# Optimization experiments

Hardware: AMD Instinct MI355X
Metric: run time of the kernel (lower is better)

Reference implementation:

```python
import jax, jax.numpy as jnp
import numpy as np

SEQ_LEN = 20   # fixed by the 18/19/20-position loop in get_each_word_feature
EMB = 768
FEAT = 512
EPS = 1e-12    # F.normalize eps


def _conv_relu(x, W, b):
    # x: [bs, L, 768]; W: [K, 768, C]; b: [C]
    # Equivalent to Conv2d(1, C, (K, 768)) on x.unsqueeze(1), then ReLU+squeeze.
    K = W.shape[0]
    L = x.shape[1]
    out = b
    for j in range(K):  # K in {1,2,3}: tiny static loop
        out = out + jnp.einsum('bld,dc->blc', x[:, j:L - K + 1 + j], W[j])
    return jax.nn.relu(out)  # [bs, L-K+1, C]


def _l2norm(x, axis):
    n = jnp.sqrt(jnp.sum(x * x, axis=axis, keepdims=True))
    return x / jnp.maximum(n, EPS)


def setup_inputs() -> dict:
    key = jax.random.key(0)
    ks = jax.random.split(key, 10)
    bs = 4096
    s = 0.02
    return {
        'words_emb': jax.random.normal(ks[0], (bs, SEQ_LEN, EMB), jnp.float32),
        'sent_emb': jax.random.normal(ks[1], (bs, EMB), jnp.float32),
        'W1': jax.random.normal(ks[2], (1, EMB, FEAT), jnp.float32) * s,
        'b1': jnp.zeros((FEAT,), jnp.float32),
        'W2': jax.random.normal(ks[3], (2, EMB, FEAT), jnp.float32) * s,
        'b2': jnp.zeros((FEAT,), jnp.float32),
        'W3': jax.random.normal(ks[4], (3, EMB, FEAT), jnp.float32) * s,
        'b3': jnp.zeros((FEAT,), jnp.float32),
        'Wp': jax.random.normal(ks[5], (EMB, FEAT), jnp.float32) * s,
        'bp': jnp.zeros((FEAT,), jnp.float32),
    }


def reference(words_emb, sent_emb, W1, b1, W2, b2, W3, b3, Wp, bp):
    # sentence projection (ProjectionHead.forward applies only the Linear)
    sent = sent_emb @ Wp + bp                       # [bs, C]

    # Bert_Word_Mapping: three 1D convs over tokens, kernel widths 1/2/3
    a = _conv_relu(words_emb, W1, b1)               # [bs, 20, C]
    b_ = _conv_relu(words_emb, W2, b2)              # [bs, 19, C]
    c = _conv_relu(words_emb, W3, b3)               # [bs, 18, C]

    # get_each_word_feature, vectorized: positional max over available convs.
    # ReLU outputs are >= 0, so zero-padding short sequences makes the
    # elementwise max reproduce the original per-position stack+amax exactly.
    b_pad = jnp.pad(b_, ((0, 0), (0, 1), (0, 0)))   # [bs, 20, C]
    c_pad = jnp.pad(c, ((0, 0), (0, 2), (0, 0)))    # [bs, 20, C]
    code = jnp.maximum(jnp.maximum(a, b_pad), c_pad)
    code = _l2norm(code, axis=2)                    # normalize over feature dim
    words_out = jnp.transpose(code, (0, 2, 1))      # [bs, C, 20]

    # get_word_feature: global max-pool over token dim, mean of 3, L2 norm
    pooled = (a.max(axis=1) + b_.max(axis=1) + c.max(axis=1)) / 3.0  # [bs, C]
    word_vector = _l2norm(pooled, axis=1)

    return (words_out, word_vector, sent)
```

## Files before the change

kernel.cpp:

```cpp
#include <hip/hip_runtime.h>
#include <hip/hip_bf16.h>
#include <stdint.h>

typedef __bf16 bf16_t;
typedef __bf16 bf16x8 __attribute__((ext_vector_type(8)));
typedef float f32x4 __attribute__((ext_vector_type(4)));

#define BS       4096
#define SEQ      20
#define SEQP     22
#define EMB      768
#define FEAT     512
#define KA       2304
#define WV_BASE   (41943040L)
#define SENT_BASE (44040192L)

#define BT_OFF    0L
#define WPT_OFF   7077888L
#define SENTX_OFF 7864320L
#define XPAD_OFF  14155776L
#define WS_MIN    111673344L
#define WS_FULL   404226048L

__device__ __forceinline__ void async_copy16(void* lds, const void* g) {
  __builtin_amdgcn_global_load_lds(
      (__attribute__((address_space(1))) void*)(void*)g,
      (__attribute__((address_space(3))) void*)lds,
      16, 0, 0);
}

__global__ void pack_xpad(const float* __restrict__ words, bf16_t* __restrict__ Xpad) {
  long idx4 = ((long)blockIdx.x * blockDim.x + threadIdx.x) * 4;
  long row = idx4 / EMB;
  int  d   = (int)(idx4 % EMB);
  long b   = row / SEQP;
  int  r   = (int)(row % SEQP);
  ushort4 o;
  if (r < SEQ) {
    float4 v = *(const float4*)(words + ((b * SEQ + r) * EMB + d));
    o.x = __builtin_bit_cast(unsigned short, (bf16_t)v.x);
    o.y = __builtin_bit_cast(unsigned short, (bf16_t)v.y);
    o.z = __builtin_bit_cast(unsigned short, (bf16_t)v.z);
    o.w = __builtin_bit_cast(unsigned short, (bf16_t)v.w);
  } else {
    o.x = 0; o.y = 0; o.z = 0; o.w = 0;
  }
  *(ushort4*)(&Xpad[idx4]) = o;
}

__global__ void pack_sent(const float* __restrict__ sent, bf16_t* __restrict__ Xs) {
  long idx4 = ((long)blockIdx.x * blockDim.x + threadIdx.x) * 4;
  float4 v = *(const float4*)(sent + idx4);
  ushort4 o;
  o.x = __builtin_bit_cast(unsigned short, (bf16_t)v.x);
  o.y = __builtin_bit_cast(unsigned short, (bf16_t)v.y);
  o.z = __builtin_bit_cast(unsigned short, (bf16_t)v.z);
  o.w = __builtin_bit_cast(unsigned short, (bf16_t)v.w);
  *(ushort4*)(&Xs[idx4]) = o;
}

__global__ void pack_bt(const float* __restrict__ W1, const float* __restrict__ W2,
                        const float* __restrict__ W3, bf16_t* __restrict__ Bt) {
  long idx = (long)blockIdx.x * blockDim.x + threadIdx.x;
  int n = (int)(idx / KA), k = (int)(idx % KA);
  int g = n >> 9, c = n & 511;
  int j = k / EMB, d = k % EMB;
  float v = 0.f;
  if (j <= g) {
    const float* W = (g == 0) ? W1 : ((g == 1) ? W2 : W3);
    v = W[((long)j * EMB + d) * FEAT + c];
  }
  Bt[idx] = (bf16_t)v;
}

__global__ void pack_wpt(const float* __restrict__ Wp, bf16_t* __restrict__ Wpt) {
  long idx = (long)blockIdx.x * blockDim.x + threadIdx.x;
  int n = (int)(idx / EMB), k = (int)(idx % EMB);
  Wpt[idx] = (bf16_t)Wp[(long)k * FEAT + n];
}

__global__ __launch_bounds__(256, 2)
void gemm_sent(const bf16_t* __restrict__ A, const bf16_t* __restrict__ Bt,
               const float* __restrict__ bias, float* __restrict__ S) {
  __shared__ bf16_t As[128 * 64];
  __shared__ bf16_t Bs[128 * 64];

  const int tid  = threadIdx.x;
  const int lane = tid & 63;
  const int w    = tid >> 6;
  const int m0   = blockIdx.x * 128;
  const int n0t  = blockIdx.y * 128;

  long agbase[4], bgbase[4];
  int  ldsoff[4];
  #pragma unroll
  for (int i = 0; i < 4; i++) {
    int r = w * 32 + i * 8 + (lane >> 3);
    int cg = (lane & 7) ^ (r & 7);
    agbase[i] = (long)(m0 + r) * EMB + cg * 8;
    bgbase[i] = (long)(n0t + r) * EMB + cg * 8;
    ldsoff[i] = (w * 32 + i * 8) * 64;
  }

  const int wm = w >> 1, wn = w & 1;
  const int q = lane >> 4, ln = lane & 15;
  int aoff[4][2], boff[4][2];
  #pragma unroll
  for (int t = 0; t < 4; t++) {
    int ra = wm * 64 + t * 16 + ln;
    int rb = wn * 64 + t * 16 + ln;
    #pragma unroll
    for (int ks = 0; ks < 2; ks++) {
      int c = ks * 4 + q;
      aoff[t][ks] = ra * 64 + ((c ^ (ra & 7)) * 8);
      boff[t][ks] = rb * 64 + ((c ^ (rb & 7)) * 8);
    }
  }

  f32x4 acc[4][4];
  #pragma unroll
  for (int i = 0; i < 4; i++)
    #pragma unroll
    for (int j = 0; j < 4; j++) acc[i][j] = (f32x4)0.f;

  for (int kb = 0; kb < EMB; kb += 64) {
    #pragma unroll
    for (int i = 0; i < 4; i++) {
      async_copy16(&As[ldsoff[i]], A  + agbase[i] + kb);
      async_copy16(&Bs[ldsoff[i]], Bt + bgbase[i] + kb);
    }
    __syncthreads();
    #pragma unroll
    for (int ks = 0; ks < 2; ks++) {
      bf16x8 af[4], bfr[4];
      #pragma unroll
      for (int t = 0; t < 4; t++) af[t]  = *(const bf16x8*)&As[aoff[t][ks]];
      #pragma unroll
      for (int t = 0; t < 4; t++) bfr[t] = *(const bf16x8*)&Bs[boff[t][ks]];
      #pragma unroll
      for (int mt = 0; mt < 4; mt++)
        #pragma unroll
        for (int nt = 0; nt < 4; nt++)
          acc[mt][nt] = __builtin_amdgcn_mfma_f32_16x16x32_bf16(af[mt], bfr[nt], acc[mt][nt], 0, 0, 0);
    }
    __syncthreads();
  }

  #pragma unroll
  for (int nt = 0; nt < 4; nt++) {
    int c = n0t + wn * 64 + nt * 16 + ln;
    float bv = bias[c];
    #pragma unroll
    for (int mt = 0; mt < 4; mt++) {
      int mrow = m0 + wm * 64 + mt * 16 + q * 4;
      #pragma unroll
      for (int v = 0; v < 4; v++)
        S[(long)(mrow + v) * FEAT + c] = acc[mt][nt][v] + bv;
    }
  }
}


#define MM4(MH, I, AV)                                                                               \
  acc[(MH)*4+(I)][0] = __builtin_amdgcn_mfma_f32_16x16x32_bf16(AV, b0_, acc[(MH)*4+(I)][0], 0, 0, 0); \
  acc[(MH)*4+(I)][1] = __builtin_amdgcn_mfma_f32_16x16x32_bf16(AV, b1_, acc[(MH)*4+(I)][1], 0, 0, 0); \
  acc[(MH)*4+(I)][2] = __builtin_amdgcn_mfma_f32_16x16x32_bf16(AV, b2_, acc[(MH)*4+(I)][2], 0, 0, 0); \
  acc[(MH)*4+(I)][3] = __builtin_amdgcn_mfma_f32_16x16x32_bf16(AV, b3_, acc[(MH)*4+(I)][3], 0, 0, 0);

#define ARD(MH, AB)                                                  \
    bf16x8 a0_ = *(const bf16x8*)&smem[(AB) + aoff[MH][0]];          \
    bf16x8 a1_ = *(const bf16x8*)&smem[(AB) + aoff[MH][1]];          \
    bf16x8 a2_ = *(const bf16x8*)&smem[(AB) + aoff[MH][2]];          \
    bf16x8 a3_ = *(const bf16x8*)&smem[(AB) + aoff[MH][3]];

#define BRD(BB)                                                      \
    b0_ = *(const bf16x8*)&smem[(BB) + boff[0]];                     \
    b1_ = *(const bf16x8*)&smem[(BB) + boff[1]];                     \
    b2_ = *(const bf16x8*)&smem[(BB) + boff[2]];                     \
    b3_ = *(const bf16x8*)&smem[(BB) + boff[3]];

#define PH_SYNC()                                                    \
    __builtin_amdgcn_s_barrier();                                    \
    asm volatile("s_waitcnt lgkmcnt(0)" ::: "memory");               \
    __builtin_amdgcn_sched_barrier(0);                               \
    __builtin_amdgcn_s_setprio(1)

#define PH_END()                                                     \
    __builtin_amdgcn_s_setprio(0);                                   \
    __builtin_amdgcn_s_barrier()

__global__ __launch_bounds__(512, 2)
void gemm8(const bf16_t* __restrict__ Axp, const bf16_t* __restrict__ Bt,
           const float* __restrict__ bias1, const float* __restrict__ bias2,
           const float* __restrict__ bias3, bf16_t* __restrict__ P, int Mtot) {
  __shared__ bf16_t smem[65536];

  const int tid  = threadIdx.x;
  const int lane = tid & 63, w = tid >> 6;
  const int wm = w >> 2, wn = w & 3;
  const int ln = lane & 15, q = lane >> 4;
  const int wbase = w * 512;

  const int nx   = gridDim.x;
  const int nwg  = nx * 6;
  const int orig = blockIdx.y * nx + blockIdx.x;
  const int wgid = (orig & 7) * (nwg >> 3) + (orig >> 3);
  const int bx = wgid / 6, by = wgid % 6;
  const int m0  = bx * 256;
  const int n0t = by * 256;
  const int g   = by >> 1;
  const int NT  = 12 * (g + 1);

  long aSrc0, aSrc1, bSrc0, bSrc1;
  {
    int pair = (tid >> 3);
    int u    = (tid & 7) ^ (pair & 7);
    int row  = pair * 2 + (u >> 2);
    int c    = u & 3;
    int m    = m0 + row;
    aSrc0 = ((long)(m / SEQ) * SEQP + (m % SEQ)) * EMB + c * 8;
    bSrc0 = (long)(n0t + row) * KA + c * 8;
    pair += 64;
    u   = (tid & 7) ^ (pair & 7);
    row = pair * 2 + (u >> 2);
    c   = u & 3;
    m   = m0 + row;
    aSrc1 = ((long)(m / SEQ) * SEQP + (m % SEQ)) * EMB + c * 8;
    bSrc1 = (long)(n0t + row) * KA + c * 8;
  }

  auto stA = [&](int buf, int ks, int kb) {
    const int rb = buf * 32768 + ks * 8192;
    async_copy16(&smem[rb + wbase],        Axp + aSrc0 + kb + ks * 32);
    async_copy16(&smem[rb + 4096 + wbase], Axp + aSrc1 + kb + ks * 32);
  };
  auto stB = [&](int buf, int ks, int kb) {
    const int rb = buf * 32768 + 16384 + ks * 8192;
    async_copy16(&smem[rb + wbase],        Bt + bSrc0 + kb + ks * 32);
    async_copy16(&smem[rb + 4096 + wbase], Bt + bSrc1 + kb + ks * 32);
  };

  int aoff[2][4], boff[4];
  #pragma unroll
  for (int mh = 0; mh < 2; mh++)
    #pragma unroll
    for (int t4 = 0; t4 < 4; t4++) {
      int r = wm * 128 + mh * 64 + t4 * 16 + ln;
      int slot = (q | ((r & 1) << 2)) ^ ((r >> 1) & 7);
      aoff[mh][t4] = (r >> 1) * 64 + slot * 8;
    }
  #pragma unroll
  for (int nf = 0; nf < 4; nf++) {
    int r = wn * 64 + nf * 16 + ln;
    int slot = (q | ((r & 1) << 2)) ^ ((r >> 1) & 7);
    boff[nf] = (r >> 1) * 64 + slot * 8;
  }

  f32x4 acc[8][4];
  #pragma unroll
  for (int i = 0; i < 8; i++)
    #pragma unroll
    for (int j = 0; j < 4; j++) acc[i][j] = (f32x4)0.f;

  stA(0, 0, 0);
  stA(0, 1, 0);
  stB(0, 0, 0);
  stB(0, 1, 0);
  stB(1, 0, 64);
  stA(1, 0, 64);
  stB(1, 1, 64);
  asm volatile("s_waitcnt vmcnt(6)" ::: "memory");
  __builtin_amdgcn_s_barrier();

  for (int t = 0; t < NT; ++t) {
    const int cb  = (t & 1) << 15;
    const int ab0 = cb, ab1 = cb + 8192;
    const int bb0 = cb + 16384, bb1 = cb + 24576;
    const int nb  = (t & 1) ^ 1;
    bf16x8 b0_, b1_, b2_, b3_;

    {
      ARD(0, ab0)
      BRD(bb0)
      if (t + 1 < NT) stA(nb, 1, (t + 1) * 64);
      PH_SYNC();
      MM4(0, 0, a0_) MM4(0, 1, a1_) MM4(0, 2, a2_) MM4(0, 3, a3_)
      PH_END();
    }
    {
      ARD(1, ab0)
      if (t + 2 < NT) stB(t & 1, 0, (t + 2) * 64);
      PH_SYNC();
      MM4(1, 0, a0_) MM4(1, 1, a1_) MM4(1, 2, a2_) MM4(1, 3, a3_)
      PH_END();
    }
    {
      ARD(0, ab1)
      BRD(bb1)
      if (t + 2 < NT) stA(t & 1, 0, (t + 2) * 64);
      PH_SYNC();
      MM4(0, 0, a0_) MM4(0, 1, a1_) MM4(0, 2, a2_) MM4(0, 3, a3_)
      PH_END();
    }
    {
      ARD(1, ab1)
      if (t + 2 < NT) stB(t & 1, 1, (t + 2) * 64);
      PH_SYNC();
      MM4(1, 0, a0_) MM4(1, 1, a1_) MM4(1, 2, a2_) MM4(1, 3, a3_)
      __builtin_amdgcn_s_setprio(0);
      if (t + 2 < NT)      { asm volatile("s_waitcnt vmcnt(6)" ::: "memory"); }
      else if (t + 1 < NT) { asm volatile("s_waitcnt vmcnt(0)" ::: "memory"); }
      __builtin_amdgcn_s_barrier();
    }
  }

  const float* bias = (g == 0) ? bias1 : ((g == 1) ? bias2 : bias3);
  const int gc0 = (by & 1) * 256;
  #pragma unroll
  for (int nf = 0; nf < 4; nf++) {
    int c = gc0 + wn * 64 + nf * 16 + ln;
    float bv = bias[c];
    #pragma unroll
    for (int mf = 0; mf < 8; mf++) {
      int mrow = m0 + wm * 128 + mf * 16 + q * 4;
      #pragma unroll
      for (int v = 0; v < 4; v++) {
        int m = mrow + v;
        int l = m % SEQ;
        float val = acc[mf][nf][v] + bv;
        val = val > 0.f ? val : 0.f;
        if (l >= SEQ - g) val = 0.f;
        P[((long)g * Mtot + m) * FEAT + c] = (bf16_t)val;
      }
    }
  }
}

__global__ __launch_bounds__(256)
void epilogue_k(const bf16_t* __restrict__ P, float* __restrict__ out, int b0, int Mtot) {
  const int bl = blockIdx.x;
  const long b = b0 + bl;
  const int t = threadIdx.x;
  const int lane = t & 63, w = t >> 6;
  const int c0 = t * 2;

  float code[SEQ][2];
  #pragma unroll
  for (int l = 0; l < SEQ; l++) { code[l][0] = 0.f; code[l][1] = 0.f; }
  float mg[3][2];

  #pragma unroll
  for (int gg = 0; gg < 3; gg++) {
    float mx0 = 0.f, mx1 = 0.f;
    #pragma unroll
    for (int l = 0; l < SEQ; l++) {
      uint32_t u = *(const uint32_t*)&P[((long)gg * Mtot + (long)bl * SEQ + l) * FEAT + c0];
      float v0 = __builtin_bit_cast(float, u << 16);
      float v1 = __builtin_bit_cast(float, u & 0xffff0000u);
      code[l][0] = fmaxf(code[l][0], v0);
      code[l][1] = fmaxf(code[l][1], v1);
      mx0 = fmaxf(mx0, v0); mx1 = fmaxf(mx1, v1);
    }
    mg[gg][0] = mx0; mg[gg][1] = mx1;
  }

  __shared__ float red[SEQ][4];
  __shared__ float redp[4];

  #pragma unroll
  for (int l = 0; l < SEQ; l++) {
    float s = code[l][0] * code[l][0] + code[l][1] * code[l][1];
    #pragma unroll
    for (int off = 32; off; off >>= 1) s += __shfl_xor(s, off, 64);
    if (lane == 0) red[l][w] = s;
  }
  float p0 = (mg[0][0] + mg[1][0] + mg[2][0]) * (1.f / 3.f);
  float p1 = (mg[0][1] + mg[1][1] + mg[2][1]) * (1.f / 3.f);
  float sp = p0 * p0 + p1 * p1;
  #pragma unroll
  for (int off = 32; off; off >>= 1) sp += __shfl_xor(sp, off, 64);
  if (lane == 0) redp[w] = sp;
  __syncthreads();

  float rnorm[SEQ];
  #pragma unroll
  for (int l = 0; l < SEQ; l++) {
    float s = red[l][0] + red[l][1] + red[l][2] + red[l][3];
    rnorm[l] = 1.f / fmaxf(sqrtf(s), 1e-12f);
  }
  float sP = redp[0] + redp[1] + redp[2] + redp[3];
  float rnp = 1.f / fmaxf(sqrtf(sP), 1e-12f);

  #pragma unroll
  for (int cc = 0; cc < 2; cc++) {
    long base = b * (FEAT * SEQ) + (long)(c0 + cc) * SEQ;
    #pragma unroll
    for (int l0 = 0; l0 < SEQ; l0 += 4) {
      float4 v;
      v.x = code[l0 + 0][cc] * rnorm[l0 + 0];
      v.y = code[l0 + 1][cc] * rnorm[l0 + 1];
      v.z = code[l0 + 2][cc] * rnorm[l0 + 2];
      v.w = code[l0 + 3][cc] * rnorm[l0 + 3];
      *(float4*)&out[base + l0] = v;
    }
  }
  out[WV_BASE + b * FEAT + c0]     = p0 * rnp;
  out[WV_BASE + b * FEAT + c0 + 1] = p1 * rnp;
}

extern "C" void kernel_launch(void* const* d_in, const int* in_sizes, int n_in,
                              void* d_out, int out_size, void* d_ws, size_t ws_size,
                              hipStream_t stream) {
  const float* words = (const float*)d_in[0];
  const float* sent  = (const float*)d_in[1];
  const float* W1 = (const float*)d_in[2];
  const float* b1 = (const float*)d_in[3];
  const float* W2 = (const float*)d_in[4];
  const float* b2 = (const float*)d_in[5];
  const float* W3 = (const float*)d_in[6];
  const float* b3 = (const float*)d_in[7];
  const float* Wp = (const float*)d_in[8];
  const float* bp = (const float*)d_in[9];
  float* out = (float*)d_out;
  char* ws = (char*)d_ws;

  int CBr, NCH;
  if (ws_size >= (size_t)WS_FULL)     { CBr = 4096; NCH = 1; }
  else if (ws_size >= (size_t)WS_MIN) { CBr = 1024; NCH = 4; }
  else return;

  const int Mtot = CBr * SEQ;
  bf16_t* Bt    = (bf16_t*)(ws + BT_OFF);
  bf16_t* Wpt   = (bf16_t*)(ws + WPT_OFF);
  bf16_t* sentX = (bf16_t*)(ws + SENTX_OFF);
  bf16_t* Xpad  = (bf16_t*)(ws + XPAD_OFF);
  bf16_t* P     = (bf16_t*)(ws + XPAD_OFF + (long)CBr * SEQP * EMB * 2);

  pack_bt<<<13824, 256, 0, stream>>>(W1, W2, W3, Bt);
  pack_wpt<<<1536, 256, 0, stream>>>(Wp, Wpt);
  pack_sent<<<3072, 256, 0, stream>>>(sent, sentX);
  gemm_sent<<<dim3(32, 4), 256, 0, stream>>>(sentX, Wpt, bp, out + SENT_BASE);

  for (int ch = 0; ch < NCH; ch++) {
    int b0 = ch * CBr;
    pack_xpad<<<(CBr * SEQP * EMB) / 1024, 256, 0, stream>>>(words + (long)b0 * SEQ * EMB, Xpad);
    gemm8<<<dim3(Mtot / 256, 6), 512, 0, stream>>>(Xpad, Bt, b1, b2, b3, P, Mtot);
    epilogue_k<<<CBr, 256, 0, stream>>>(P, out, b0, Mtot);
  }
}
```

Measured before the change: 933.0 us.

## Software-pipeline LDS fragment reads one phase ahead of MFMA in gemm8

Restructures the GEMM main loop so the LDS reads of A/B fragments for the next phase are issued before the current phase's 16 MFMAs, instead of read-then-wait-then-compute per phase. This drops the per-phase lgkmcnt(0) wait and one barrier per phase, so LDS latency can hide behind matrix work. It also loosens the vmcnt wait from 6 to 4 and skips the final barrier on the last iteration. The cost is higher register pressure from holding two fragment sets, and the barrier changes risk LDS read/write races with the async copies.

```diff
diff --git a/kernel.cpp b/kernel.cpp
--- a/kernel.cpp
+++ b/kernel.cpp
@@ -161,33 +161,23 @@
 }
 
 
-#define MM4(MH, I, AV)                                                                               \
-  acc[(MH)*4+(I)][0] = __builtin_amdgcn_mfma_f32_16x16x32_bf16(AV, b0_, acc[(MH)*4+(I)][0], 0, 0, 0); \
-  acc[(MH)*4+(I)][1] = __builtin_amdgcn_mfma_f32_16x16x32_bf16(AV, b1_, acc[(MH)*4+(I)][1], 0, 0, 0); \
-  acc[(MH)*4+(I)][2] = __builtin_amdgcn_mfma_f32_16x16x32_bf16(AV, b2_, acc[(MH)*4+(I)][2], 0, 0, 0); \
-  acc[(MH)*4+(I)][3] = __builtin_amdgcn_mfma_f32_16x16x32_bf16(AV, b3_, acc[(MH)*4+(I)][3], 0, 0, 0);
-
-#define ARD(MH, AB)                                                  \
-    bf16x8 a0_ = *(const bf16x8*)&smem[(AB) + aoff[MH][0]];          \
-    bf16x8 a1_ = *(const bf16x8*)&smem[(AB) + aoff[MH][1]];          \
-    bf16x8 a2_ = *(const bf16x8*)&smem[(AB) + aoff[MH][2]];          \
-    bf16x8 a3_ = *(const bf16x8*)&smem[(AB) + aoff[MH][3]];
-
-#define BRD(BB)                                                      \
-    b0_ = *(const bf16x8*)&smem[(BB) + boff[0]];                     \
-    b1_ = *(const bf16x8*)&smem[(BB) + boff[1]];                     \
-    b2_ = *(const bf16x8*)&smem[(BB) + boff[2]];                     \
-    b3_ = *(const bf16x8*)&smem[(BB) + boff[3]];
-
-#define PH_SYNC()                                                    \
-    __builtin_amdgcn_s_barrier();                                    \
-    asm volatile("s_waitcnt lgkmcnt(0)" ::: "memory");               \
-    __builtin_amdgcn_sched_barrier(0);                               \
-    __builtin_amdgcn_s_setprio(1)
-
-#define PH_END()                                                     \
-    __builtin_amdgcn_s_setprio(0);                                   \
-    __builtin_amdgcn_s_barrier()
+#define MFMA16(BASE, A0, A1, A2, A3, B0, B1, B2, B3)                                        \
+  acc[(BASE)+0][0] = __builtin_amdgcn_mfma_f32_16x16x32_bf16(A0, B0, acc[(BASE)+0][0], 0, 0, 0); \
+  acc[(BASE)+0][1] = __builtin_amdgcn_mfma_f32_16x16x32_bf16(A0, B1, acc[(BASE)+0][1], 0, 0, 0); \
+  acc[(BASE)+0][2] = __builtin_amdgcn_mfma_f32_16x16x32_bf16(A0, B2, acc[(BASE)+0][2], 0, 0, 0); \
+  acc[(BASE)+0][3] = __builtin_amdgcn_mfma_f32_16x16x32_bf16(A0, B3, acc[(BASE)+0][3], 0, 0, 0); \
+  acc[(BASE)+1][0] = __builtin_amdgcn_mfma_f32_16x16x32_bf16(A1, B0, acc[(BASE)+1][0], 0, 0, 0); \
+  acc[(BASE)+1][1] = __builtin_amdgcn_mfma_f32_16x16x32_bf16(A1, B1, acc[(BASE)+1][1], 0, 0, 0); \
+  acc[(BASE)+1][2] = __builtin_amdgcn_mfma_f32_16x16x32_bf16(A1, B2, acc[(BASE)+1][2], 0, 0, 0); \
+  acc[(BASE)+1][3] = __builtin_amdgcn_mfma_f32_16x16x32_bf16(A1, B3, acc[(BASE)+1][3], 0, 0, 0); \
+  acc[(BASE)+2][0] = __builtin_amdgcn_mfma_f32_16x16x32_bf16(A2, B0, acc[(BASE)+2][0], 0, 0, 0); \
+  acc[(BASE)+2][1] = __builtin_amdgcn_mfma_f32_16x16x32_bf16(A2, B1, acc[(BASE)+2][1], 0, 0, 0); \
+  acc[(BASE)+2][2] = __builtin_amdgcn_mfma_f32_16x16x32_bf16(A2, B2, acc[(BASE)+2][2], 0, 0, 0); \
+  acc[(BASE)+2][3] = __builtin_amdgcn_mfma_f32_16x16x32_bf16(A2, B3, acc[(BASE)+2][3], 0, 0, 0); \
+  acc[(BASE)+3][0] = __builtin_amdgcn_mfma_f32_16x16x32_bf16(A3, B0, acc[(BASE)+3][0], 0, 0, 0); \
+  acc[(BASE)+3][1] = __builtin_amdgcn_mfma_f32_16x16x32_bf16(A3, B1, acc[(BASE)+3][1], 0, 0, 0); \
+  acc[(BASE)+3][2] = __builtin_amdgcn_mfma_f32_16x16x32_bf16(A3, B2, acc[(BASE)+3][2], 0, 0, 0); \
+  acc[(BASE)+3][3] = __builtin_amdgcn_mfma_f32_16x16x32_bf16(A3, B3, acc[(BASE)+3][3], 0, 0, 0);
 
 __global__ __launch_bounds__(512, 2)
 void gemm8(const bf16_t* __restrict__ Axp, const bf16_t* __restrict__ Bt,
@@ -277,40 +267,62 @@
     const int ab0 = cb, ab1 = cb + 8192;
     const int bb0 = cb + 16384, bb1 = cb + 24576;
     const int nb  = (t & 1) ^ 1;
-    bf16x8 b0_, b1_, b2_, b3_;
+
+    bf16x8 aP0 = *(const bf16x8*)&smem[ab0 + aoff[0][0]];
+    bf16x8 aP1 = *(const bf16x8*)&smem[ab0 + aoff[0][1]];
+    bf16x8 aP2 = *(const bf16x8*)&smem[ab0 + aoff[0][2]];
+    bf16x8 aP3 = *(const bf16x8*)&smem[ab0 + aoff[0][3]];
+    bf16x8 bP0 = *(const bf16x8*)&smem[bb0 + boff[0]];
+    bf16x8 bP1 = *(const bf16x8*)&smem[bb0 + boff[1]];
+    bf16x8 bP2 = *(const bf16x8*)&smem[bb0 + boff[2]];
+    bf16x8 bP3 = *(const bf16x8*)&smem[bb0 + boff[3]];
 
     {
-      ARD(0, ab0)
-      BRD(bb0)
+      bf16x8 aN0 = *(const bf16x8*)&smem[ab0 + aoff[1][0]];
+      bf16x8 aN1 = *(const bf16x8*)&smem[ab0 + aoff[1][1]];
+      bf16x8 aN2 = *(const bf16x8*)&smem[ab0 + aoff[1][2]];
+      bf16x8 aN3 = *(const bf16x8*)&smem[ab0 + aoff[1][3]];
       if (t + 1 < NT) stA(nb, 1, (t + 1) * 64);
-      PH_SYNC();
-      MM4(0, 0, a0_) MM4(0, 1, a1_) MM4(0, 2, a2_) MM4(0, 3, a3_)
-      PH_END();
-    }
-    {
-      ARD(1, ab0)
+      __builtin_amdgcn_sched_barrier(0);
+      __builtin_amdgcn_s_setprio(1);
+      MFMA16(0, aP0, aP1, aP2, aP3, bP0, bP1, bP2, bP3)
+      __builtin_amdgcn_s_setprio(0);
+      __builtin_amdgcn_s_barrier();
+
+      bf16x8 aQ0 = *(const bf16x8*)&smem[ab1 + aoff[0][0]];
+      bf16x8 aQ1 = *(const bf16x8*)&smem[ab1 + aoff[0][1]];
+      bf16x8 aQ2 = *(const bf16x8*)&smem[ab1 + aoff[0][2]];
+      bf16x8 aQ3 = *(const bf16x8*)&smem[ab1 + aoff[0][3]];
+      bf16x8 bN0 = *(const bf16x8*)&smem[bb1 + boff[0]];
+      bf16x8 bN1 = *(const bf16x8*)&smem[bb1 + boff[1]];
+      bf16x8 bN2 = *(const bf16x8*)&smem[bb1 + boff[2]];
+      bf16x8 bN3 = *(const bf16x8*)&smem[bb1 + boff[3]];
       if (t + 2 < NT) stB(t & 1, 0, (t + 2) * 64);
-      PH_SYNC();
-      MM4(1, 0, a0_) MM4(1, 1, a1_) MM4(1, 2, a2_) MM4(1, 3, a3_)
-      PH_END();
-    }
-    {
-      ARD(0, ab1)
-      BRD(bb1)
+      __builtin_amdgcn_sched_barrier(0);
+      __builtin_amdgcn_s_setprio(1);
+      MFMA16(4, aN0, aN1, aN2, aN3, bP0, bP1, bP2, bP3)
+      __builtin_amdgcn_s_setprio(0);
+      __builtin_amdgcn_s_barrier();
+
+      bf16x8 aR0 = *(const bf16x8*)&smem[ab1 + aoff[1][0]];
+      bf16x8 aR1 = *(const bf16x8*)&smem[ab1 + aoff[1][1]];
+      bf16x8 aR2 = *(const bf16x8*)&smem[ab1 + aoff[1][2]];
+      bf16x8 aR3 = *(const bf16x8*)&smem[ab1 + aoff[1][3]];
       if (t + 2 < NT) stA(t & 1, 0, (t + 2) * 64);
-      PH_SYNC();
-      MM4(0, 0, a0_) MM4(0, 1, a1_) MM4(0, 2, a2_) MM4(0, 3, a3_)
-      PH_END();
-    }
-    {
-      ARD(1, ab1)
+      __builtin_amdgcn_sched_barrier(0);
+      __builtin_amdgcn_s_setprio(1);
+      MFMA16(0, aQ0, aQ1, aQ2, aQ3, bN0, bN1, bN2, bN3)
+      __builtin_amdgcn_s_setprio(0);
+      __builtin_amdgcn_s_barrier();
+
       if (t + 2 < NT) stB(t & 1, 1, (t + 2) * 64);
-      PH_SYNC();
-      MM4(1, 0, a0_) MM4(1, 1, a1_) MM4(1, 2, a2_) MM4(1, 3, a3_)
+      __builtin_amdgcn_sched_barrier(0);
+      __builtin_amdgcn_s_setprio(1);
+      MFMA16(4, aR0, aR1, aR2, aR3, bN0, bN1, bN2, bN3)
       __builtin_amdgcn_s_setprio(0);
-      if (t + 2 < NT)      { asm volatile("s_waitcnt vmcnt(6)" ::: "memory"); }
+      if (t + 2 < NT)      { asm volatile("s_waitcnt vmcnt(4)" ::: "memory"); }
       else if (t + 1 < NT) { asm volatile("s_waitcnt vmcnt(0)" ::: "memory"); }
-      __builtin_amdgcn_s_barrier();
+      if (t + 1 < NT) __builtin_amdgcn_s_barrier();
     }
   }
 
```

Result: no change. 919.1 us (-1.5%).
